# Kernel tuning notes

Hardware: AMD Instinct MI355X
Metric: run time of the kernel (lower is better)

Reference implementation:

```python
import jax, jax.numpy as jnp
from jax import lax
import numpy as np

HIDDEN = 32
IN_CH = 128   # observation_space.n + 1
OUT_DIM = 8   # action_space.n


def setup_inputs() -> dict:
    key = jax.random.key(0)
    ks = jax.random.split(key, 7)
    B, T = 512, 512
    s = 1.0 / np.sqrt(HIDDEN)  # PyTorch RNN init scale U(-1/sqrt(H), 1/sqrt(H))
    seq = jax.random.normal(ks[0], (B, T, IN_CH), dtype=jnp.float32)
    W_ih = jax.random.uniform(ks[1], (HIDDEN, IN_CH), minval=-s, maxval=s, dtype=jnp.float32)
    W_hh = jax.random.uniform(ks[2], (HIDDEN, HIDDEN), minval=-s, maxval=s, dtype=jnp.float32)
    b_ih = jax.random.uniform(ks[3], (HIDDEN,), minval=-s, maxval=s, dtype=jnp.float32)
    b_hh = jax.random.uniform(ks[4], (HIDDEN,), minval=-s, maxval=s, dtype=jnp.float32)
    s2 = 1.0 / np.sqrt(HIDDEN)
    W_fc = jax.random.uniform(ks[5], (OUT_DIM, HIDDEN), minval=-s2, maxval=s2, dtype=jnp.float32)
    b_fc = jax.random.uniform(ks[6], (OUT_DIM,), minval=-s2, maxval=s2, dtype=jnp.float32)
    return {"seq": seq, "W_ih": W_ih, "W_hh": W_hh, "b_ih": b_ih,
            "b_hh": b_hh, "W_fc": W_fc, "b_fc": b_fc}


def reference(seq, W_ih, W_hh, b_ih, b_hh, W_fc, b_fc):
    # seq: [B, T, I]. Precompute input projection once (big GEMM),
    # then scan the 32-wide ReLU recurrence over time.
    B = seq.shape[0]
    xp = jnp.einsum('bti,hi->bth', seq, W_ih) + (b_ih + b_hh)  # [B, T, H]
    xp_t = jnp.swapaxes(xp, 0, 1)  # [T, B, H]
    h0 = jnp.zeros((B, HIDDEN), dtype=seq.dtype)

    def step(h, x_t):
        h = jax.nn.relu(x_t + h @ W_hh.T)
        return h, None

    h_last, _ = lax.scan(step, h0, xp_t)  # h_last: [B, H] (last timestep)
    return h_last @ W_fc.T + b_fc  # [B, OUT_DIM]
```

## Files before the change

kernel.cpp:

```cpp
#include <hip/hip_runtime.h>

#define HID   32
#define INCH  128
#define OUTD  8
#define BATCH 512
#define TLEN  512
#define TT    32
#define NCHUNK (TLEN / TT)

typedef __attribute__((ext_vector_type(2)))  float  f32x2;
typedef __attribute__((ext_vector_type(4)))  float  vf4;
typedef __attribute__((ext_vector_type(8)))  short  short8_t;
typedef __attribute__((ext_vector_type(16))) float  f32x16_t;

__device__ __forceinline__ void split8(const float4 f0, const float4 f1,
                                       short8_t* hi, short8_t* lo)
{
    float x[8] = {f0.x, f0.y, f0.z, f0.w, f1.x, f1.y, f1.z, f1.w};
    short8_t h, l;
    #pragma unroll
    for (int e = 0; e < 8; ++e) {
        const unsigned u  = __float_as_uint(x[e]);
        const unsigned hb = u & 0xFFFF0000u;
        h[e] = (short)(u >> 16);
        const float r = x[e] - __uint_as_float(hb);
        l[e] = (short)(__float_as_uint(r) >> 16);
    }
    *hi = h; *lo = l;
}

__global__ __launch_bounds__(128, 1) void rnn_fused_kernel(
    const float* __restrict__ seq, const float* __restrict__ Wih,
    const float* __restrict__ Whh, const float* __restrict__ bih,
    const float* __restrict__ bhh, const float* __restrict__ Wfc,
    const float* __restrict__ bfc, float* __restrict__ out)
{
    __shared__ __align__(16) float xpb[2][TT * HID];
    __shared__ __align__(16) float hlds[64];

    const int tid  = threadIdx.x;
    const int wid  = tid >> 6;
    const int l    = tid & 63;
    const int row  = blockIdx.x;

    if (wid == 0) {
        const int ch = l & 31;
        f32x2 w2[16];
        {
            const vf4* W4 = (const vf4*)(Whh + ch * HID);
            #pragma unroll
            for (int q = 0; q < 8; ++q) {
                const vf4 t = W4[q];
                w2[2 * q + 0] = t.xy;
                w2[2 * q + 1] = t.zw;
            }
        }
        hlds[l] = 0.0f;
        const vf4* h4 = (const vf4*)&hlds[(l >> 5) * 32];

        __builtin_amdgcn_s_setprio(1);
        for (int c = 0; c < NCHUNK; ++c) {
            __syncthreads();
            const float* xb = xpb[c & 1];
            float xv = xb[ch];
            #pragma unroll
            for (int tt = 0; tt < TT; ++tt) {
                const float xvn = (tt < TT - 1) ? xb[(tt + 1) * HID + ch] : 0.0f;
                f32x2 a0 = {xv, 0.0f};
                f32x2 a1 = {0.0f, 0.0f}, a2 = {0.0f, 0.0f}, a3 = {0.0f, 0.0f};
                #pragma unroll
                for (int q = 0; q < 8; ++q) {
                    const vf4 hq = h4[q];
                    a0 = w2[2 * q + 0] * hq.xy + a0;
                    a1 = w2[2 * q + 1] * hq.zw + a1;
                    const f32x2 t0 = a0; a0 = a2; a2 = t0;
                    const f32x2 t1 = a1; a1 = a3; a3 = t1;
                }
                const f32x2 s01 = a0 + a1;
                const f32x2 s23 = a2 + a3;
                const f32x2 s = s01 + s23;
                const float h = fmaxf(s.x + s.y, 0.0f);
                hlds[l] = h;
                xv = xvn;
            }
        }
        __builtin_amdgcn_s_setprio(0);

        if (l < OUTD) {
            float s = bfc[l];
            #pragma unroll
            for (int j = 0; j < HID; ++j)
                s = fmaf(hlds[j], Wfc[l * HID + j], s);
            out[row * OUTD + l] = s;
        }
    } else {
        const int trow  = l & 31;
        const int khalf = l >> 5;
        const int irow  = l & 31;

        short8_t whi[8], wlo[8];
        #pragma unroll
        for (int kb = 0; kb < 8; ++kb) {
            const float* wp = Wih + irow * INCH + kb * 16 + khalf * 8;
            const float4 f0 = *(const float4*)(wp);
            const float4 f1 = *(const float4*)(wp + 4);
            split8(f0, f1, &whi[kb], &wlo[kb]);
        }
        const float biasv = bih[irow] + bhh[irow];

        for (int c = 0; c < NCHUNK; ++c) {
            const float* sp = seq +
                ((size_t)row * TLEN + (size_t)c * TT + trow) * INCH + khalf * 8;
            short8_t ahi[8], alo[8];
            #pragma unroll
            for (int kb = 0; kb < 8; ++kb) {
                const float4 f0 = *(const float4*)(sp + kb * 16);
                const float4 f1 = *(const float4*)(sp + kb * 16 + 4);
                split8(f0, f1, &ahi[kb], &alo[kb]);
            }

            f32x16_t acc;
            #pragma unroll
            for (int r2 = 0; r2 < 16; ++r2) acc[r2] = biasv;
            #pragma unroll
            for (int kb = 0; kb < 8; ++kb) {
                acc = __builtin_amdgcn_mfma_f32_32x32x16_bf16(ahi[kb], whi[kb], acc, 0, 0, 0);
                acc = __builtin_amdgcn_mfma_f32_32x32x16_bf16(ahi[kb], wlo[kb], acc, 0, 0, 0);
                acc = __builtin_amdgcn_mfma_f32_32x32x16_bf16(alo[kb], whi[kb], acc, 0, 0, 0);
            }

            float* xb = xpb[c & 1];
            #pragma unroll
            for (int r2 = 0; r2 < 16; ++r2) {
                const int tp = (r2 & 3) + 8 * (r2 >> 2) + 4 * khalf;
                xb[tp * HID + irow] = acc[r2];
            }
            __syncthreads();
        }
    }
}

extern "C" void kernel_launch(void* const* d_in, const int* in_sizes, int n_in,
                              void* d_out, int out_size, void* d_ws, size_t ws_size,
                              hipStream_t stream) {
    const float* seq = (const float*)d_in[0];
    const float* Wih = (const float*)d_in[1];
    const float* Whh = (const float*)d_in[2];
    const float* bih = (const float*)d_in[3];
    const float* bhh = (const float*)d_in[4];
    const float* Wfc = (const float*)d_in[5];
    const float* bfc = (const float*)d_in[6];

    rnn_fused_kernel<<<dim3(BATCH), dim3(128), 0, stream>>>(
        seq, Wih, Whh, bih, bhh, Wfc, bfc, (float*)d_out);
}
```

Before: 59.04 us.

## Split recurrent dot product across wave halves and transpose xp buffer

```diff
diff --git a/kernel.cpp b/kernel.cpp
--- a/kernel.cpp
+++ b/kernel.cpp
@@ -12,6 +12,18 @@
 typedef __attribute__((ext_vector_type(4)))  float  vf4;
 typedef __attribute__((ext_vector_type(8)))  short  short8_t;
 typedef __attribute__((ext_vector_type(16))) float  f32x16_t;
+typedef __attribute__((ext_vector_type(2)))  int    i32x2;
+
+__device__ __forceinline__ float half_combine(float p)
+{
+#if __has_builtin(__builtin_amdgcn_permlane32_swap)
+    i32x2 r = __builtin_amdgcn_permlane32_swap(
+        __float_as_int(p), __float_as_int(p), false, false);
+    return __int_as_float(r[0]) + __int_as_float(r[1]);
+#else
+    return p + __shfl_xor(p, 32, 64);
+#endif
+}
 
 __device__ __forceinline__ void split8(const float4 f0, const float4 f1,
                                        short8_t* hi, short8_t* lo)
@@ -44,44 +56,54 @@
     const int row  = blockIdx.x;
 
     if (wid == 0) {
-        const int ch = l & 31;
-        f32x2 w2[16];
+        const int ch    = l & 31;
+        const int half  = l >> 5;
+        const int jbase = half * 16;
+        const int m     = 4 * (ch & 7);
+
+        f32x2 w2[8];
         {
-            const vf4* W4 = (const vf4*)(Whh + ch * HID);
+            const vf4* W4 = (const vf4*)(Whh + ch * HID + jbase);
             #pragma unroll
-            for (int q = 0; q < 8; ++q) {
+            for (int q = 0; q < 4; ++q) {
                 const vf4 t = W4[q];
                 w2[2 * q + 0] = t.xy;
                 w2[2 * q + 1] = t.zw;
             }
         }
+
         hlds[l] = 0.0f;
-        const vf4* h4 = (const vf4*)&hlds[(l >> 5) * 32];
+        const vf4* h4 = (const vf4*)&hlds[half * 48];
 
         __builtin_amdgcn_s_setprio(1);
         for (int c = 0; c < NCHUNK; ++c) {
             __syncthreads();
-            const float* xb = xpb[c & 1];
-            float xv = xb[ch];
+            const float* xb = xpb[c & 1] + ch * TT;
+            vf4 xq[8];
+            xq[0] = *(const vf4*)(xb + (0 ^ m));
+
             #pragma unroll
             for (int tt = 0; tt < TT; ++tt) {
-                const float xvn = (tt < TT - 1) ? xb[(tt + 1) * HID + ch] : 0.0f;
-                f32x2 a0 = {xv, 0.0f};
-                f32x2 a1 = {0.0f, 0.0f}, a2 = {0.0f, 0.0f}, a3 = {0.0f, 0.0f};
-                #pragma unroll
-                for (int q = 0; q < 8; ++q) {
-                    const vf4 hq = h4[q];
-                    a0 = w2[2 * q + 0] * hq.xy + a0;
-                    a1 = w2[2 * q + 1] * hq.zw + a1;
-                    const f32x2 t0 = a0; a0 = a2; a2 = t0;
-                    const f32x2 t1 = a1; a1 = a3; a3 = t1;
-                }
-                const f32x2 s01 = a0 + a1;
-                const f32x2 s23 = a2 + a3;
-                const f32x2 s = s01 + s23;
-                const float h = fmaxf(s.x + s.y, 0.0f);
-                hlds[l] = h;
-                xv = xvn;
+                const float xv = xq[tt >> 2][tt & 3];
+                const vf4 h0 = h4[0];
+                const vf4 h1 = h4[1];
+                const vf4 h2 = h4[2];
+                const vf4 h3 = h4[3];
+                f32x2 a0 = w2[0] * h0.xy;
+                f32x2 a1 = w2[1] * h0.zw;
+                a0 = w2[2] * h1.xy + a0;
+                a1 = w2[3] * h1.zw + a1;
+                a0 = w2[4] * h2.xy + a0;
+                a1 = w2[5] * h2.zw + a1;
+                a0 = w2[6] * h3.xy + a0;
+                a1 = w2[7] * h3.zw + a1;
+                const f32x2 s2 = a0 + a1;
+                const float p = s2.x + s2.y;
+                const float tot = half_combine(p);
+                const float hn = fmaxf(xv + tot, 0.0f);
+                hlds[l] = hn;
+                if (tt < 7)
+                    xq[tt + 1] = *(const vf4*)(xb + (((tt + 1) * 4) ^ m));
             }
         }
         __builtin_amdgcn_s_setprio(0);
@@ -107,6 +129,7 @@
             split8(f0, f1, &whi[kb], &wlo[kb]);
         }
         const float biasv = bih[irow] + bhh[irow];
+        const int m2 = 4 * (irow & 7);
 
         for (int c = 0; c < NCHUNK; ++c) {
             const float* sp = seq +
@@ -129,11 +152,14 @@
                 acc = __builtin_amdgcn_mfma_f32_32x32x16_bf16(alo[kb], whi[kb], acc, 0, 0, 0);
             }
 
-            float* xb = xpb[c & 1];
+            float* xbT = xpb[c & 1] + irow * TT;
             #pragma unroll
-            for (int r2 = 0; r2 < 16; ++r2) {
-                const int tp = (r2 & 3) + 8 * (r2 >> 2) + 4 * khalf;
-                xb[tp * HID + irow] = acc[r2];
+            for (int g = 0; g < 4; ++g) {
+                const int t0 = 8 * g + 4 * khalf;
+                vf4 v;
+                v.x = acc[4 * g + 0]; v.y = acc[4 * g + 1];
+                v.z = acc[4 * g + 2]; v.w = acc[4 * g + 3];
+                *(vf4*)(xbT + (t0 ^ m2)) = v;
             }
             __syncthreads();
         }
```

Result: faster. 53.29 us (-9.8%).

## Keep recurrent hidden state in registers using DPP rotations and permlane reductions

Applied to the files above, without the earlier changes.

```diff
diff --git a/kernel.cpp b/kernel.cpp
--- a/kernel.cpp
+++ b/kernel.cpp
@@ -8,10 +8,43 @@
 #define TT    32
 #define NCHUNK (TLEN / TT)
 
+#define XSTRIDE 68
+
 typedef __attribute__((ext_vector_type(2)))  float  f32x2;
 typedef __attribute__((ext_vector_type(4)))  float  vf4;
 typedef __attribute__((ext_vector_type(8)))  short  short8_t;
 typedef __attribute__((ext_vector_type(16))) float  f32x16_t;
+typedef __attribute__((ext_vector_type(2)))  int    i32x2;
+
+#define ROR_CTRL(N) (0x120 | (N))
+
+#define RORF(v, N) __int_as_float(__builtin_amdgcn_update_dpp(              \
+    0, __float_as_int(v), ROR_CTRL(N), 0xF, 0xF, true))
+
+#define UPDF(old, src, N, rmask) __int_as_float(__builtin_amdgcn_update_dpp(\
+    __float_as_int(old), __float_as_int(src), ROR_CTRL(N), (rmask), 0xF, false))
+
+__device__ __forceinline__ float swap32_add(float p)
+{
+#if __has_builtin(__builtin_amdgcn_permlane32_swap)
+    i32x2 r = __builtin_amdgcn_permlane32_swap(
+        __float_as_int(p), __float_as_int(p), false, false);
+    return __int_as_float(r[0]) + __int_as_float(r[1]);
+#else
+    return p + __shfl_xor(p, 32, 64);
+#endif
+}
+
+__device__ __forceinline__ float swap16_add(float p)
+{
+#if __has_builtin(__builtin_amdgcn_permlane16_swap)
+    i32x2 r = __builtin_amdgcn_permlane16_swap(
+        __float_as_int(p), __float_as_int(p), false, false);
+    return __int_as_float(r[0]) + __int_as_float(r[1]);
+#else
+    return p + __shfl_xor(p, 16, 64);
+#endif
+}
 
 __device__ __forceinline__ void split8(const float4 f0, const float4 f1,
                                        short8_t* hi, short8_t* lo)
@@ -35,8 +68,8 @@
     const float* __restrict__ bhh, const float* __restrict__ Wfc,
     const float* __restrict__ bfc, float* __restrict__ out)
 {
-    __shared__ __align__(16) float xpb[2][TT * HID];
-    __shared__ __align__(16) float hlds[64];
+    __shared__ __align__(16) float xlds[2][16 * XSTRIDE];
+    __shared__ __align__(16) float hlds[HID];
 
     const int tid  = threadIdx.x;
     const int wid  = tid >> 6;
@@ -44,48 +77,60 @@
     const int row  = blockIdx.x;
 
     if (wid == 0) {
-        const int ch = l & 31;
-        f32x2 w2[16];
-        {
-            const vf4* W4 = (const vf4*)(Whh + ch * HID);
-            #pragma unroll
-            for (int q = 0; q < 8; ++q) {
-                const vf4 t = W4[q];
-                w2[2 * q + 0] = t.xy;
-                w2[2 * q + 1] = t.zw;
-            }
-        }
-        hlds[l] = 0.0f;
-        const vf4* h4 = (const vf4*)&hlds[(l >> 5) * 32];
+        const int g = l >> 4;
+        const int q = l & 15;
+
+        f32x2 w2[2][4];
+        #pragma unroll
+        for (int cc = 0; cc < 2; ++cc)
+            #pragma unroll
+            for (int s = 0; s < 4; ++s) {
+                const int jp = (q - 4 * g - s) & 15;
+                w2[cc][s] = *(const f32x2*)(Whh + (2 * q + cc) * HID + 2 * jp);
+            }
+
+        float hA = 0.0f, hB = 0.0f;
 
         __builtin_amdgcn_s_setprio(1);
         for (int c = 0; c < NCHUNK; ++c) {
             __syncthreads();
-            const float* xb = xpb[c & 1];
-            float xv = xb[ch];
+            const float* xt = xlds[c & 1] + q * XSTRIDE;
+            vf4 xq[16];
+            #pragma unroll
+            for (int u = 0; u < 16; ++u) xq[u] = *(const vf4*)(xt + 4 * u);
+
             #pragma unroll
             for (int tt = 0; tt < TT; ++tt) {
-                const float xvn = (tt < TT - 1) ? xb[(tt + 1) * HID + ch] : 0.0f;
-                f32x2 a0 = {xv, 0.0f};
-                f32x2 a1 = {0.0f, 0.0f}, a2 = {0.0f, 0.0f}, a3 = {0.0f, 0.0f};
-                #pragma unroll
-                for (int q = 0; q < 8; ++q) {
-                    const vf4 hq = h4[q];
-                    a0 = w2[2 * q + 0] * hq.xy + a0;
-                    a1 = w2[2 * q + 1] * hq.zw + a1;
-                    const f32x2 t0 = a0; a0 = a2; a2 = t0;
-                    const f32x2 t1 = a1; a1 = a3; a3 = t1;
-                }
-                const f32x2 s01 = a0 + a1;
-                const f32x2 s23 = a2 + a3;
-                const f32x2 s = s01 + s23;
-                const float h = fmaxf(s.x + s.y, 0.0f);
-                hlds[l] = h;
-                xv = xvn;
+                const float xv0 = (tt & 1) ? xq[tt >> 1].z : xq[tt >> 1].x;
+                const float xv1 = (tt & 1) ? xq[tt >> 1].w : xq[tt >> 1].y;
+                f32x2 h2; h2.x = hA; h2.y = hB;
+                f32x2 a0 = w2[0][0] * h2;
+                f32x2 a1 = w2[1][0] * h2;
+                f32x2 hs;
+                hs.x = RORF(hA, 1); hs.y = RORF(hB, 1);
+                a0 = w2[0][1] * hs + a0;  a1 = w2[1][1] * hs + a1;
+                hs.x = RORF(hA, 2); hs.y = RORF(hB, 2);
+                a0 = w2[0][2] * hs + a0;  a1 = w2[1][2] * hs + a1;
+                hs.x = RORF(hA, 3); hs.y = RORF(hB, 3);
+                a0 = w2[0][3] * hs + a0;  a1 = w2[1][3] * hs + a1;
+                float p0 = a0.x + a0.y;
+                float p1 = a1.x + a1.y;
+                p0 = swap16_add(p0);  p1 = swap16_add(p1);
+                p0 = swap32_add(p0);  p1 = swap32_add(p1);
+                const float y0 = fmaxf(p0 + xv0, 0.0f);
+                const float y1 = fmaxf(p1 + xv1, 0.0f);
+                const float tA = UPDF(y0, y0, 8, 0xC);
+                hA = UPDF(tA, tA, 4, 0xA);
+                const float tB = UPDF(y1, y1, 8, 0xC);
+                hB = UPDF(tB, tB, 4, 0xA);
             }
         }
         __builtin_amdgcn_s_setprio(0);
 
+        if (g == 0) {
+            f32x2 hp; hp.x = hA; hp.y = hB;
+            *(f32x2*)&hlds[2 * q] = hp;
+        }
         if (l < OUTD) {
             float s = bfc[l];
             #pragma unroll
@@ -129,11 +174,11 @@
                 acc = __builtin_amdgcn_mfma_f32_32x32x16_bf16(alo[kb], whi[kb], acc, 0, 0, 0);
             }
 
-            float* xb = xpb[c & 1];
+            float* xb = xlds[c & 1];
             #pragma unroll
             for (int r2 = 0; r2 < 16; ++r2) {
-                const int tp = (r2 & 3) + 8 * (r2 >> 2) + 4 * khalf;
-                xb[tp * HID + irow] = acc[r2];
+                const int m = (r2 & 3) + 8 * (r2 >> 2) + 4 * khalf;
+                xb[(irow >> 1) * XSTRIDE + 2 * m + (irow & 1)] = acc[r2];
             }
             __syncthreads();
         }
```

After: 61.59 us. +4.3%, slower.

## Split into producer/consumer mega-kernel with MFMA recurrence over 32-row batch groups

Applied to the files above, without the earlier changes.

```diff
diff --git a/kernel.cpp b/kernel.cpp
--- a/kernel.cpp
+++ b/kernel.cpp
@@ -5,13 +5,44 @@
 #define OUTD  8
 #define BATCH 512
 #define TLEN  512
-#define TT    32
-#define NCHUNK (TLEN / TT)
-
-typedef __attribute__((ext_vector_type(2)))  float  f32x2;
-typedef __attribute__((ext_vector_type(4)))  float  vf4;
+#define NGRP  16
+#define NCHK  32
+#define ITEMS 2048
+#define XP_BYTES (16u * 1024u * 1024u)
+
+typedef __attribute__((ext_vector_type(2)))  int    i32x2;
+typedef __attribute__((ext_vector_type(4)))  int    i32x4;
 typedef __attribute__((ext_vector_type(8)))  short  short8_t;
 typedef __attribute__((ext_vector_type(16))) float  f32x16_t;
+typedef __attribute__((ext_vector_type(8)))  _Float16 half8_t;
+typedef __attribute__((ext_vector_type(2)))  _Float16 h2v;
+
+__device__ __forceinline__ i32x2 swap32v(int a, int b)
+{
+#if __has_builtin(__builtin_amdgcn_permlane32_swap)
+    return __builtin_amdgcn_permlane32_swap(a, b, false, false);
+#else
+    const int lane = threadIdx.x & 63;
+    int as = __shfl_xor(a, 32, 64), bs = __shfl_xor(b, 32, 64);
+    i32x2 r;
+    r[0] = (lane < 32) ? bs : a;
+    r[1] = (lane < 32) ? b  : as;
+    return r;
+#endif
+}
+
+__device__ __forceinline__ float swap32_add(float p)
+{
+    i32x2 r = swap32v(__float_as_int(p), __float_as_int(p));
+    return __int_as_float(r[0]) + __int_as_float(r[1]);
+}
+
+__device__ __forceinline__ int bhalf(int x, int p, int from)
+{
+    const int z = (p == from) ? x : 0;
+    i32x2 r = swap32v(z, z);
+    return r[0] + r[1];
+}
 
 __device__ __forceinline__ void split8(const float4 f0, const float4 f1,
                                        short8_t* hi, short8_t* lo)
@@ -29,113 +60,231 @@
     *hi = h; *lo = l;
 }
 
-__global__ __launch_bounds__(128, 1) void rnn_fused_kernel(
+__device__ __forceinline__ unsigned pk2_rn(float a, float b)
+{
+    unsigned short ha = __builtin_bit_cast(unsigned short, (_Float16)a);
+    unsigned short hb = __builtin_bit_cast(unsigned short, (_Float16)b);
+    return (unsigned)ha | ((unsigned)hb << 16);
+}
+
+__device__ __forceinline__ unsigned cvt_relu_pk(float a, float b)
+{
+    const float ra = fmaxf(a, 0.0f);
+    const float rb = fmaxf(b, 0.0f);
+#if __has_builtin(__builtin_amdgcn_cvt_pkrtz)
+    return __builtin_bit_cast(unsigned, __builtin_amdgcn_cvt_pkrtz(ra, rb));
+#else
+    return pk2_rn(ra, rb);
+#endif
+}
+
+__device__ __forceinline__ float2 unpk2(unsigned u)
+{
+    h2v h = __builtin_bit_cast(h2v, u);
+    return make_float2((float)h[0], (float)h[1]);
+}
+
+__global__ __launch_bounds__(256, 2) void rnn_mega_kernel(
     const float* __restrict__ seq, const float* __restrict__ Wih,
     const float* __restrict__ Whh, const float* __restrict__ bih,
     const float* __restrict__ bhh, const float* __restrict__ Wfc,
-    const float* __restrict__ bfc, float* __restrict__ out)
-{
-    __shared__ __align__(16) float xpb[2][TT * HID];
-    __shared__ __align__(16) float hlds[64];
-
-    const int tid  = threadIdx.x;
-    const int wid  = tid >> 6;
-    const int l    = tid & 63;
-    const int row  = blockIdx.x;
-
-    if (wid == 0) {
-        const int ch = l & 31;
-        f32x2 w2[16];
-        {
-            const vf4* W4 = (const vf4*)(Whh + ch * HID);
+    const float* __restrict__ bfc, float* __restrict__ out,
+    char* __restrict__ ws)
+{
+    int* ready = (int*)(ws + XP_BYTES);
+    int* qctr  = (int*)(ws + XP_BYTES + 4096);
+
+    if (blockIdx.x < NGRP) {
+        if (threadIdx.x >= 64) return;
+        const int g = blockIdx.x;
+        const int l = threadIdx.x;
+        const int p = l >> 5;
+
+        half8_t wfA, wfB;
+        #pragma unroll
+        for (int e = 0; e < 8; ++e) {
+            wfA[e] = (_Float16)Whh[(l & 31) * HID + 8 * p + e];
+            wfB[e] = (_Float16)Whh[(l & 31) * HID + 16 + 8 * p + e];
+        }
+
+        i32x4 hAw = {0, 0, 0, 0}, hBw = {0, 0, 0, 0};
+        f32x16_t Dl;
+        #pragma unroll
+        for (int r = 0; r < 16; ++r) Dl[r] = 0.0f;
+
+        const char* xpg = ws + (size_t)g * (TLEN * 2048) + (size_t)l * 32;
+
+        while (__hip_atomic_load(&ready[g * 32 + 0], __ATOMIC_RELAXED,
+                                 __HIP_MEMORY_SCOPE_AGENT) < 4)
+            __builtin_amdgcn_s_sleep(2);
+        __builtin_amdgcn_fence(__ATOMIC_ACQUIRE, "agent");
+
+        i32x4 P0a = *(const i32x4*)(xpg + 0 * 2048);
+        i32x4 P0b = *(const i32x4*)(xpg + 0 * 2048 + 16);
+        i32x4 P1a = *(const i32x4*)(xpg + 1 * 2048);
+        i32x4 P1b = *(const i32x4*)(xpg + 1 * 2048 + 16);
+        i32x4 P2a = *(const i32x4*)(xpg + 2 * 2048);
+        i32x4 P2b = *(const i32x4*)(xpg + 2 * 2048 + 16);
+        i32x4 P3a = *(const i32x4*)(xpg + 3 * 2048);
+        i32x4 P3b = *(const i32x4*)(xpg + 3 * 2048 + 16);
+
+        __builtin_amdgcn_s_setprio(1);
+
+#define STEP(PA, PB, T)                                                       \
+        {                                                                     \
+            f32x16_t Cv;                                                      \
+            float2 f;                                                         \
+            f = unpk2((unsigned)PA[0]); Cv[0]  = f.x; Cv[1]  = f.y;           \
+            f = unpk2((unsigned)PA[1]); Cv[2]  = f.x; Cv[3]  = f.y;           \
+            f = unpk2((unsigned)PA[2]); Cv[4]  = f.x; Cv[5]  = f.y;           \
+            f = unpk2((unsigned)PA[3]); Cv[6]  = f.x; Cv[7]  = f.y;           \
+            f = unpk2((unsigned)PB[0]); Cv[8]  = f.x; Cv[9]  = f.y;           \
+            f = unpk2((unsigned)PB[1]); Cv[10] = f.x; Cv[11] = f.y;           \
+            f = unpk2((unsigned)PB[2]); Cv[12] = f.x; Cv[13] = f.y;           \
+            f = unpk2((unsigned)PB[3]); Cv[14] = f.x; Cv[15] = f.y;           \
+            if ((T) + 4 < TLEN) {                                             \
+                PA = *(const i32x4*)(xpg + ((size_t)((T) + 4)) * 2048);       \
+                PB = *(const i32x4*)(xpg + ((size_t)((T) + 4)) * 2048 + 16);  \
+            }                                                                 \
+            f32x16_t U = __builtin_amdgcn_mfma_f32_32x32x16_f16(              \
+                wfB, __builtin_bit_cast(half8_t, hBw), Cv, 0, 0, 0);          \
+            Dl = __builtin_amdgcn_mfma_f32_32x32x16_f16(                      \
+                wfA, __builtin_bit_cast(half8_t, hAw), U, 0, 0, 0);           \
+            const int w0 = (int)cvt_relu_pk(Dl[0],  Dl[1]);                   \
+            const int w1 = (int)cvt_relu_pk(Dl[2],  Dl[3]);                   \
+            const int w2 = (int)cvt_relu_pk(Dl[4],  Dl[5]);                   \
+            const int w3 = (int)cvt_relu_pk(Dl[6],  Dl[7]);                   \
+            const int w4 = (int)cvt_relu_pk(Dl[8],  Dl[9]);                   \
+            const int w5 = (int)cvt_relu_pk(Dl[10], Dl[11]);                  \
+            const int w6 = (int)cvt_relu_pk(Dl[12], Dl[13]);                  \
+            const int w7 = (int)cvt_relu_pk(Dl[14], Dl[15]);                  \
+                         \
+            const int b02 = bhalf(w2, p, 0);               \
+            const int b03 = bhalf(w3, p, 0);                                  \
+            const int b10 = bhalf(w0, p, 1);               \
+            const int b11 = bhalf(w1, p, 1);                                  \
+            const int b06 = bhalf(w6, p, 0);                                  \
+            const int b07 = bhalf(w7, p, 0);                                  \
+            const int b14 = bhalf(w4, p, 1);                                  \
+            const int b15 = bhalf(w5, p, 1);                                  \
+            hAw[0] = p ? b02 : w0;                            \
+            hAw[1] = p ? b03 : w1;                            \
+            hAw[2] = p ? w2  : b10;                           \
+            hAw[3] = p ? w3  : b11;                           \
+            hBw[0] = p ? b06 : w4;                         \
+            hBw[1] = p ? b07 : w5;                                            \
+            hBw[2] = p ? w6  : b14;                                           \
+            hBw[3] = p ? w7  : b15;                                           \
+        }
+
+        for (int c = 0; c < NCHK; ++c) {
+            const int cn = (c + 1 < NCHK) ? c + 1 : c;
+            while (__hip_atomic_load(&ready[g * 32 + cn], __ATOMIC_RELAXED,
+                                     __HIP_MEMORY_SCOPE_AGENT) < 4)
+                __builtin_amdgcn_s_sleep(2);
+            __builtin_amdgcn_fence(__ATOMIC_ACQUIRE, "agent");
+
+            for (int tq = 0; tq < 4; ++tq) {
+                const int tb = c * 16 + tq * 4;
+                STEP(P0a, P0b, tb + 0)
+                STEP(P1a, P1b, tb + 1)
+                STEP(P2a, P2b, tb + 2)
+                STEP(P3a, P3b, tb + 3)
+            }
+        }
+#undef STEP
+        __builtin_amdgcn_s_setprio(0);
+
+        float hr[16];
+        #pragma unroll
+        for (int r = 0; r < 16; ++r) hr[r] = fmaxf(Dl[r], 0.0f);
+
+        float po[8];
+        #pragma unroll
+        for (int o = 0; o < OUTD; ++o) {
+            float s = 0.0f;
             #pragma unroll
-            for (int q = 0; q < 8; ++q) {
-                const vf4 t = W4[q];
-                w2[2 * q + 0] = t.xy;
-                w2[2 * q + 1] = t.zw;
+            for (int r = 0; r < 16; ++r) {
+                const int i = (r & 3) + 8 * (r >> 2) + 4 * p;
+                s = fmaf(hr[r], Wfc[o * HID + i], s);
             }
-        }
-        hlds[l] = 0.0f;
-        const vf4* h4 = (const vf4*)&hlds[(l >> 5) * 32];
-
-        __builtin_amdgcn_s_setprio(1);
-        for (int c = 0; c < NCHUNK; ++c) {
+            po[o] = swap32_add(s) + bfc[o];
+        }
+        if (l < 32) {
+            float4 v0 = make_float4(po[0], po[1], po[2], po[3]);
+            float4 v1 = make_float4(po[4], po[5], po[6], po[7]);
+            float* op = out + (size_t)(g * 32 + l) * OUTD;
+            *(float4*)op = v0;
+            *(float4*)(op + 4) = v1;
+        }
+    } else {
+        __shared__ int s_item;
+        const int tid = threadIdx.x;
+        const int wv  = tid >> 6;
+        const int l   = tid & 63;
+        const int p   = l >> 5;
+
+        short8_t whi[8], wlo[8];
+        #pragma unroll
+        for (int kb = 0; kb < 8; ++kb) {
+            const float* wp = Wih + (l & 31) * INCH + kb * 16 + p * 8;
+            split8(*(const float4*)wp, *(const float4*)(wp + 4),
+                   &whi[kb], &wlo[kb]);
+        }
+        float biasr[16];
+        #pragma unroll
+        for (int r = 0; r < 16; ++r) {
+            const int i = (r & 3) + 8 * (r >> 2) + 4 * p;
+            biasr[r] = bih[i] + bhh[i];
+        }
+
+        while (true) {
+            if (tid == 0)
+                s_item = __hip_atomic_fetch_add(qctr, 1, __ATOMIC_RELAXED,
+                                                __HIP_MEMORY_SCOPE_AGENT);
             __syncthreads();
-            const float* xb = xpb[c & 1];
-            float xv = xb[ch];
+            const int item = s_item;
+            if (item >= ITEMS) break;
+
+            const int c   = item >> 6;
+            const int g   = (item >> 2) & 15;
+            const int sub = item & 3;
+            const int t   = c * 16 + sub * 4 + wv;
+
+            const float* sp = seq +
+                ((size_t)(g * 32 + (l & 31)) * TLEN + t) * INCH + p * 8;
+
+            f32x16_t acc;
             #pragma unroll
-            for (int tt = 0; tt < TT; ++tt) {
-                const float xvn = (tt < TT - 1) ? xb[(tt + 1) * HID + ch] : 0.0f;
-                f32x2 a0 = {xv, 0.0f};
-                f32x2 a1 = {0.0f, 0.0f}, a2 = {0.0f, 0.0f}, a3 = {0.0f, 0.0f};
-                #pragma unroll
-                for (int q = 0; q < 8; ++q) {
-                    const vf4 hq = h4[q];
-                    a0 = w2[2 * q + 0] * hq.xy + a0;
-                    a1 = w2[2 * q + 1] * hq.zw + a1;
-                    const f32x2 t0 = a0; a0 = a2; a2 = t0;
-                    const f32x2 t1 = a1; a1 = a3; a3 = t1;
-                }
-                const f32x2 s01 = a0 + a1;
-                const f32x2 s23 = a2 + a3;
-                const f32x2 s = s01 + s23;
-                const float h = fmaxf(s.x + s.y, 0.0f);
-                hlds[l] = h;
-                xv = xvn;
-            }
-        }
-        __builtin_amdgcn_s_setprio(0);
-
-        if (l < OUTD) {
-            float s = bfc[l];
-            #pragma unroll
-            for (int j = 0; j < HID; ++j)
-                s = fmaf(hlds[j], Wfc[l * HID + j], s);
-            out[row * OUTD + l] = s;
-        }
-    } else {
-        const int trow  = l & 31;
-        const int khalf = l >> 5;
-        const int irow  = l & 31;
-
-        short8_t whi[8], wlo[8];
-        #pragma unroll
-        for (int kb = 0; kb < 8; ++kb) {
-            const float* wp = Wih + irow * INCH + kb * 16 + khalf * 8;
-            const float4 f0 = *(const float4*)(wp);
-            const float4 f1 = *(const float4*)(wp + 4);
-            split8(f0, f1, &whi[kb], &wlo[kb]);
-        }
-        const float biasv = bih[irow] + bhh[irow];
-
-        for (int c = 0; c < NCHUNK; ++c) {
-            const float* sp = seq +
-                ((size_t)row * TLEN + (size_t)c * TT + trow) * INCH + khalf * 8;
-            short8_t ahi[8], alo[8];
+            for (int r = 0; r < 16; ++r) acc[r] = biasr[r];
+
             #pragma unroll
             for (int kb = 0; kb < 8; ++kb) {
-                const float4 f0 = *(const float4*)(sp + kb * 16);
-                const float4 f1 = *(const float4*)(sp + kb * 16 + 4);
-                split8(f0, f1, &ahi[kb], &alo[kb]);
+                short8_t shi, slo;
+                split8(*(const float4*)(sp + kb * 16),
+                       *(const float4*)(sp + kb * 16 + 4), &shi, &slo);
+                acc = __builtin_amdgcn_mfma_f32_32x32x16_bf16(whi[kb], shi, acc, 0, 0, 0);
+                acc = __builtin_amdgcn_mfma_f32_32x32x16_bf16(whi[kb], slo, acc, 0, 0, 0);
+                acc = __builtin_amdgcn_mfma_f32_32x32x16_bf16(wlo[kb], shi, acc, 0, 0, 0);
             }
 
-            f32x16_t acc;
-            #pragma unroll
-            for (int r2 = 0; r2 < 16; ++r2) acc[r2] = biasv;
-            #pragma unroll
-            for (int kb = 0; kb < 8; ++kb) {
-                acc = __builtin_amdgcn_mfma_f32_32x32x16_bf16(ahi[kb], whi[kb], acc, 0, 0, 0);
-                acc = __builtin_amdgcn_mfma_f32_32x32x16_bf16(ahi[kb], wlo[kb], acc, 0, 0, 0);
-                acc = __builtin_amdgcn_mfma_f32_32x32x16_bf16(alo[kb], whi[kb], acc, 0, 0, 0);
-            }
-
-            float* xb = xpb[c & 1];
-            #pragma unroll
-            for (int r2 = 0; r2 < 16; ++r2) {
-                const int tp = (r2 & 3) + 8 * (r2 >> 2) + 4 * khalf;
-                xb[tp * HID + irow] = acc[r2];
-            }
+            i32x4 oa, ob;
+            oa[0] = (int)pk2_rn(acc[0],  acc[1]);
+            oa[1] = (int)pk2_rn(acc[2],  acc[3]);
+            oa[2] = (int)pk2_rn(acc[4],  acc[5]);
+            oa[3] = (int)pk2_rn(acc[6],  acc[7]);
+            ob[0] = (int)pk2_rn(acc[8],  acc[9]);
+            ob[1] = (int)pk2_rn(acc[10], acc[11]);
+            ob[2] = (int)pk2_rn(acc[12], acc[13]);
+            ob[3] = (int)pk2_rn(acc[14], acc[15]);
+            char* dst = ws + ((size_t)(g * TLEN + t) * 64 + l) * 32;
+            *(i32x4*)dst = oa;
+            *(i32x4*)(dst + 16) = ob;
+
             __syncthreads();
+            if (tid == 0)
+                __hip_atomic_fetch_add(&ready[g * 32 + c], 1, __ATOMIC_RELEASE,
+                                       __HIP_MEMORY_SCOPE_AGENT);
         }
     }
 }
@@ -151,6 +300,8 @@
     const float* Wfc = (const float*)d_in[5];
     const float* bfc = (const float*)d_in[6];
 
-    rnn_fused_kernel<<<dim3(BATCH), dim3(128), 0, stream>>>(
-        seq, Wih, Whh, bih, bhh, Wfc, bfc, (float*)d_out);
-}
+    (void)hipMemsetAsync((char*)d_ws + XP_BYTES, 0, 8192, stream);
+
+    rnn_mega_kernel<<<dim3(512), dim3(256), 0, stream>>>(
+        seq, Wih, Whh, bih, bhh, Wfc, bfc, (float*)d_out, (char*)d_ws);
+}
```

Result: slower. 213.3 us (+261.2%).
